# Kernel tuning notes

Measured on AMD Instinct MI355X. Metric: run time of the kernel, lower is better.

Reference implementation:

```python
import jax, jax.numpy as jnp
import numpy as np

B, H, Wd, CIN = 4, 64, 64, 65   # batch, height, width, in_channels (incl. time)
COUT = 256                      # out_channels (incl. time)
K = 3
KK = K * K
PAD, STRIDE = 1, 1
SOUT = 4                        # output_stabilizer_size (C4 rotations)
CURV = 1.0                      # Lorentz manifold curvature k
LIN_FEAT = (CIN - 1) * KK + 1   # 577


def make_c4_z2_indices(ksize):
    # (out_rotation, in_stabilizer=1, u, v, [s, u_src, v_src]) index table,
    # realizing the C4 filter rotation as a gather (as in GrouPy).
    f = np.arange(ksize * ksize).reshape(ksize, ksize)
    inds = np.zeros((4, 1, ksize, ksize, 3), dtype=np.int64)
    for r in range(4):
        rot = np.rot90(f, r)
        u, v = np.unravel_index(rot, (ksize, ksize))
        inds[r, 0, :, :, 1] = u
        inds[r, 0, :, :, 2] = v
    return inds

INDS = make_c4_z2_indices(K)


def setup_inputs() -> dict:
    key = jax.random.key(0)
    k1, k2, k3 = jax.random.split(key, 3)
    stdv = float(np.sqrt(2.0 / ((CIN - 1) * KK)))  # reset_parameters
    x = jax.random.normal(k1, (B, H, Wd, CIN), dtype=jnp.float32)
    W = jax.random.uniform(k2, (COUT, LIN_FEAT), minval=-stdv, maxval=stdv, dtype=jnp.float32)
    b = jax.random.uniform(k3, (COUT,), minval=-stdv, maxval=stdv, dtype=jnp.float32)
    return {"x": x, "W": W, "b": b}


def _unfold(x):
    # x: (B, C, H, W) -> (B, C*KK, Ho*Wo) in torch.nn.Unfold layout (channel-major, kernel-minor)
    xp = jnp.pad(x, ((0, 0), (0, 0), (PAD, PAD), (PAD, PAD)))
    ho = (H + 2 * PAD - K) // STRIDE + 1
    wo = (Wd + 2 * PAD - K) // STRIDE + 1
    cols = [xp[:, :, i:i + ho * STRIDE:STRIDE, j:j + wo * STRIDE:STRIDE]
            for i in range(K) for j in range(K)]
    p = jnp.stack(cols, axis=2)  # (B, C, KK, ho, wo)
    return p.reshape(B, CIN * KK, ho * wo), ho, wo


def _forward(x, W, b):
    # torch code does x.view(B, C, H, W) on channel-last data: a reshape, not a permute.
    xv = x.reshape(B, CIN, H, Wd)
    patches, ho, wo = _unfold(xv)
    patches = jnp.transpose(patches, (0, 2, 1))          # (B, P, C*KK)
    P = patches.shape[1]
    patches = patches.reshape(B, P, CIN, 1, K, K)
    patches = jnp.broadcast_to(patches, (B, P, CIN, SOUT, K, K))  # repeat over group dim
    # --- group-equivariant filter transform realized as a gather on patches ---
    ir = INDS.reshape(-1, 3)                              # (SOUT*KK, 3)
    pi = patches[:, :, :, ir[:, 0], ir[:, 1], ir[:, 2]]   # (B, P, C, SOUT*KK)
    pi = pi.reshape(B, P, CIN, SOUT, KK)
    pt = jnp.transpose(pi, (3, 0, 1, 2, 4)).reshape(SOUT, B, P, CIN * KK)
    # --- extract_lorentz_patches (vectorized over group dim) ---
    sqrt_k = jnp.sqrt(jnp.float32(CURV))
    t = jnp.maximum(pt[..., :KK], sqrt_k)                 # clamp time components
    t_resc = jnp.sqrt(jnp.sum(t * t, axis=-1, keepdims=True) - (KK - 1) * CURV)
    sp = pt[..., KK:]                                     # (SOUT,B,P,(C-1)*KK) channel-major
    sp = sp.reshape(SOUT, B, P, CIN - 1, KK).swapaxes(-1, -2).reshape(SOUT, B, P, (CIN - 1) * KK)
    pre = jnp.concatenate([t_resc, sp], axis=-1)          # (SOUT,B,P,LIN_FEAT)
    # --- LorentzFullyConnected: linear, then recompute time from space norm ---
    y = jnp.einsum('gbpf,of->gbpo', pre, W) + b           # (SOUT,B,P,COUT)
    y_sp = y[..., 1:]
    y_t = jnp.sqrt(jnp.sum(y_sp * y_sp, axis=-1, keepdims=True) + CURV)
    out = jnp.concatenate([y_t, y_sp], axis=-1)
    out = jnp.transpose(out, (1, 0, 2, 3)).reshape(B, SOUT, ho, wo, COUT)
    return out


def reference(x, W, b):
    return _forward(x, W, b)
```

## Files before the change

kernel.cpp:

```cpp
#include <hip/hip_runtime.h>
#include <hip/hip_bf16.h>

#define CIN 65
#define LIN 577
#define NSTEP 18
#define M_  16384

typedef __bf16 bf16x8 __attribute__((ext_vector_type(8)));
typedef float  f32x4  __attribute__((ext_vector_type(4)));
typedef unsigned short u16x8 __attribute__((ext_vector_type(8)));

__constant__ int SIG[4][9] = {
  {0,1,2,3,4,5,6,7,8},
  {2,5,8,1,4,7,0,3,6},
  {8,7,6,5,4,3,2,1,0},
  {6,3,0,7,4,1,8,5,2}};

__device__ __forceinline__ int swzm(int r) { return (r ^ (r >> 2)) & 3; }

__global__ __launch_bounds__(512) void prep_k(const float* __restrict__ x,
                                              const float* __restrict__ W,
                                              __hip_bfloat16* __restrict__ A,
                                              __hip_bfloat16* __restrict__ Wg,
                                              float* __restrict__ T) {
  __shared__ float lds[CIN * 3 * 72];
  const int tid = threadIdx.x;
  if (blockIdx.x >= 256) {
    int pidx = (blockIdx.x - 256) * 512 + tid;
    int jc  = pidx & 3;
    int col = (pidx >> 2) & 255;
    int t   = pidx >> 10;
    int ks  = t % NSTEP, g = t / NSTEP;
    int k   = SIG[(4 - g) & 3][ks >> 1];
    const float* src = W + col * LIN + 1 + k * 64 + (ks & 1) * 32 + jc * 8;
    u16x8 pk;
#pragma unroll
    for (int e = 0; e < 8; ++e) {
      union { __hip_bfloat16 h; unsigned short u; } cv;
      cv.h = __float2bfloat16(src[e]);
      pk[e] = cv.u;
    }
    *(u16x8*)(Wg + (size_t)pidx * 8) = pk;
    return;
  }
  const int b = blockIdx.x >> 6, py = blockIdx.x & 63;
  const float* xb = x + (size_t)b * (CIN * 4096);
  for (int i = tid; i < CIN * 3 * 18; i += 512)
    *(f32x4*)&lds[i * 4] = (f32x4){0.f, 0.f, 0.f, 0.f};
  __syncthreads();
  for (int i = tid; i < CIN * 3 * 16; i += 512) {
    int pr = i >> 4, j = i & 15;
    int c = pr / 3, dy = pr - c * 3;
    int hy = py + dy - 1;
    if (hy >= 0 && hy < 64)
      *(f32x4*)&lds[c * 216 + dy * 72 + 4 + j * 4] =
          *(const f32x4*)(xb + c * 4096 + hy * 64 + j * 4);
  }
  __syncthreads();

  const int wave = tid >> 6, px = tid & 63;
  const int rowid = (blockIdx.x << 6) | px;
#pragma unroll
  for (int qi = 0; qi < 9; ++qi) {
    int q = wave * 9 + qi;
    int m = q >> 3, cb8 = q & 7;
    int dy = m / 3, dx = m - dy * 3;
    const float* src = &lds[(1 + cb8 * 8) * 216 + dy * 72 + 3 + dx + px];
    u16x8 pk;
#pragma unroll
    for (int e = 0; e < 8; ++e) {
      union { __hip_bfloat16 h; unsigned short u; } cv;
      cv.h = __float2bfloat16(src[e * 216]);
      pk[e] = cv.u;
    }
    *(u16x8*)(A + ((size_t)q * M_ + rowid) * 8) = pk;
  }
  if (wave == 0) {
    float s = 0.f;
#pragma unroll
    for (int m = 0; m < 9; ++m) {
      float t = fmaxf(lds[(m / 3) * 72 + 3 + (m % 3) + px], 1.f);
      s += t * t;
    }
    T[rowid] = sqrtf(s - 8.f);
  }
}

__device__ __forceinline__ void async_cp16(const void* g, void* ldsbase) {
  __builtin_amdgcn_global_load_lds(
      (const __attribute__((address_space(1))) void*)g,
      (__attribute__((address_space(3))) void*)ldsbase, 16, 0, 0);
}

__global__ __launch_bounds__(512, 4) void gemm_k(const __hip_bfloat16* __restrict__ A,
                                                 const __hip_bfloat16* __restrict__ Wg,
                                                 const float* __restrict__ W,
                                                 const float* __restrict__ bias,
                                                 const float* __restrict__ T,
                                                 float* __restrict__ out) {
  __shared__ __align__(16) char smem[51712];
  const int fid = blockIdx.x;
  const int lid = ((fid & 7) << 6) | (fid >> 3);
  const int g = lid & 3, rb = lid >> 2;
  const int brow = rb << 7;
  const int tid = threadIdx.x, wave = tid >> 6, lane = tid & 63;
  const int fr = lane & 15, fq = lane >> 4;
  const int wr = (wave >> 2) * 64, wcb = (wave & 3) * 64;

  float* Tsh = (float*)(smem + 49152);
  float* Ps  = (float*)(smem + 49664);
  if (tid < 128) Tsh[tid] = T[brow + tid];

  const int bcol0 = tid >> 2, blc0 = (tid & 3) ^ swzm(bcol0);
  const int bcol1 = 128 + (tid >> 2), blc1 = (tid & 3) ^ swzm(bcol1);
  const __hip_bfloat16* Wgg = Wg + ((size_t)(g * NSTEP) << 13);
  auto STAGE_B = [&](char* pb, int ks) {
    const __hip_bfloat16* bs = Wgg + ((size_t)ks << 13);
    async_cp16(bs + bcol0 * 32 + blc0 * 8, pb + wave * 1024);
    async_cp16(bs + bcol1 * 32 + blc1 * 8, pb + wave * 1024 + 8192);
  };

  const __hip_bfloat16* Arow = A + (((size_t)fq * M_ + brow + wr + fr) << 3);
  auto LOAD_A = [&](bf16x8* dst, int ks) {
#pragma unroll
    for (int i = 0; i < 4; ++i)
      dst[i] = *(const bf16x8*)(Arow + (size_t)ks * (M_ * 32) + i * 128);
  };

  f32x4 acc[4][4] = {};
  auto COMPUTE = [&](const char* Bb, const bf16x8* af) {
    bf16x8 bf[4];
#pragma unroll
    for (int j = 0; j < 4; ++j) {
      int c = wcb + j * 16 + fr;
      bf[j] = *(const bf16x8*)(Bb + c * 64 + ((fq ^ swzm(c)) << 4));
    }
    __builtin_amdgcn_s_setprio(1);
#pragma unroll
    for (int i = 0; i < 4; ++i)
#pragma unroll
      for (int j = 0; j < 4; ++j)
        acc[i][j] = __builtin_amdgcn_mfma_f32_16x16x32_bf16(af[i], bf[j], acc[i][j], 0, 0, 0);
    __builtin_amdgcn_s_setprio(0);
  };

  bf16x8 afA[4], afB[4];
  char *cB = smem, *nB = smem + 16384, *tB = smem + 32768;
  STAGE_B(cB, 0);
  STAGE_B(nB, 1);
  LOAD_A(afA, 0);

  for (int kp = 0; kp < NSTEP; kp += 2) {
    asm volatile("s_waitcnt vmcnt(6)" ::: "memory");
    __builtin_amdgcn_s_barrier();
    if (kp + 2 < NSTEP) STAGE_B(tB, kp + 2);
    LOAD_A(afB, kp + 1);
    COMPUTE(cB, afA);
    { char* r = cB; cB = nB; nB = tB; tB = r; }
    if (kp + 1 < NSTEP - 1) {
      asm volatile("s_waitcnt vmcnt(6)" ::: "memory");
    } else {
      asm volatile("s_waitcnt vmcnt(4)" ::: "memory");
    }
    __builtin_amdgcn_s_barrier();
    if (kp + 3 < NSTEP) STAGE_B(tB, kp + 3);
    if (kp + 2 < NSTEP) LOAD_A(afA, kp + 2);
    COMPUTE(cB, afB);
    { char* r = cB; cB = nB; nB = tB; tB = r; }
  }
  __syncthreads();

  float bo[4], w0v[4]; int oc[4];
#pragma unroll
  for (int j = 0; j < 4; ++j) {
    oc[j]  = wcb + j * 16 + fr;
    bo[j]  = bias[oc[j]];
    w0v[j] = W[oc[j] * LIN];
  }
#pragma unroll
  for (int i = 0; i < 4; ++i) {
#pragma unroll
    for (int rr = 0; rr < 4; ++rr) {
      int rl = wr + i * 16 + fq * 4 + rr;
      int row = brow + rl;
      size_t obase = ((size_t)(((row >> 12) * 4 + g) * 4096 + (row & 4095)) << 8);
      float tval = Tsh[rl];
      float s = 0.f;
#pragma unroll
      for (int j = 0; j < 4; ++j) {
        float y = acc[i][j][rr] + bo[j] + tval * w0v[j];
        if (oc[j] != 0) { s += y * y; out[obase + oc[j]] = y; }
      }
      s += __shfl_xor(s, 1); s += __shfl_xor(s, 2);
      s += __shfl_xor(s, 4); s += __shfl_xor(s, 8);
      if (fr == 0) Ps[rl * 4 + (wave & 3)] = s;
    }
  }
  __syncthreads();
  if (tid < 128) {
    int row = brow + tid;
    float s = Ps[tid * 4] + Ps[tid * 4 + 1] + Ps[tid * 4 + 2] + Ps[tid * 4 + 3] + 1.0f;
    out[(size_t)(((row >> 12) * 4 + g) * 4096 + (row & 4095)) << 8] = sqrtf(s);
  }
}

extern "C" void kernel_launch(void* const* d_in, const int* in_sizes, int n_in,
                              void* d_out, int out_size, void* d_ws, size_t ws_size,
                              hipStream_t stream) {
  const float* x    = (const float*)d_in[0];
  const float* W    = (const float*)d_in[1];
  const float* bias = (const float*)d_in[2];
  float* out = (float*)d_out;

  char* ws = (char*)d_ws;
  __hip_bfloat16* Wg = (__hip_bfloat16*)ws;
  float*          T  = (float*)(ws + 1179648);
  __hip_bfloat16* A  = (__hip_bfloat16*)(ws + 1245184);

  prep_k<<<400, 512, 0, stream>>>(x, W, A, Wg, T);
  gemm_k<<<512, 512, 0, stream>>>(A, Wg, W, bias, T, out);
}
```

Before: 43.86 us.

## Shrink GEMM tile to 64 rows with 256-thread blocks and double buffering

Restructures the GEMM kernel from 128x256 tiles with 8 waves and triple-buffered B to 64x256 tiles with 4 waves, double-buffered B and a simpler single-step loop. The grid doubles to 1024 blocks in a plain group-major order without the previous block-index swizzle, and T is read from global memory instead of staged in LDS. The aim is more blocks and occupancy with less LDS per block, at the cost of reloading B twice as often per row and exposing more A-load latency because A is no longer prefetched a step ahead.

```diff
diff --git a/kernel.cpp b/kernel.cpp
--- a/kernel.cpp
+++ b/kernel.cpp
@@ -92,43 +92,40 @@
       (__attribute__((address_space(3))) void*)ldsbase, 16, 0, 0);
 }
 
-__global__ __launch_bounds__(512, 4) void gemm_k(const __hip_bfloat16* __restrict__ A,
+__global__ __launch_bounds__(256, 4) void gemm_k(const __hip_bfloat16* __restrict__ A,
                                                  const __hip_bfloat16* __restrict__ Wg,
                                                  const float* __restrict__ W,
                                                  const float* __restrict__ bias,
                                                  const float* __restrict__ T,
                                                  float* __restrict__ out) {
-  __shared__ __align__(16) char smem[51712];
-  const int fid = blockIdx.x;
-  const int lid = ((fid & 7) << 6) | (fid >> 3);
-  const int g = lid & 3, rb = lid >> 2;
-  const int brow = rb << 7;
+  __shared__ __align__(16) char smem[32768];
+  const int g = blockIdx.x >> 8, rb = blockIdx.x & 255;
+  const int brow = rb << 6;
   const int tid = threadIdx.x, wave = tid >> 6, lane = tid & 63;
   const int fr = lane & 15, fq = lane >> 4;
-  const int wr = (wave >> 2) * 64, wcb = (wave & 3) * 64;
-
-  float* Tsh = (float*)(smem + 49152);
-  float* Ps  = (float*)(smem + 49664);
-  if (tid < 128) Tsh[tid] = T[brow + tid];
-
-  const int bcol0 = tid >> 2, blc0 = (tid & 3) ^ swzm(bcol0);
-  const int bcol1 = 128 + (tid >> 2), blc1 = (tid & 3) ^ swzm(bcol1);
+  const int wcb = wave * 64;
+
+  const int bc  = tid >> 2;
   const __hip_bfloat16* Wgg = Wg + ((size_t)(g * NSTEP) << 13);
   auto STAGE_B = [&](char* pb, int ks) {
     const __hip_bfloat16* bs = Wgg + ((size_t)ks << 13);
-    async_cp16(bs + bcol0 * 32 + blc0 * 8, pb + wave * 1024);
-    async_cp16(bs + bcol1 * 32 + blc1 * 8, pb + wave * 1024 + 8192);
+#pragma unroll
+    for (int l = 0; l < 4; ++l) {
+      int c = l * 64 + bc;
+      int lc = (tid & 3) ^ swzm(c);
+      async_cp16(bs + c * 32 + lc * 8, pb + (l * 256 + wave * 64) * 16);
+    }
   };
-
-  const __hip_bfloat16* Arow = A + (((size_t)fq * M_ + brow + wr + fr) << 3);
-  auto LOAD_A = [&](bf16x8* dst, int ks) {
+  const __hip_bfloat16* Alane = A + (((size_t)fq * M_ + brow + fr) << 3);
+  bf16x8 af[4];
+  auto LOAD_A = [&](int ks) {
 #pragma unroll
     for (int i = 0; i < 4; ++i)
-      dst[i] = *(const bf16x8*)(Arow + (size_t)ks * (M_ * 32) + i * 128);
+      af[i] = *(const bf16x8*)(Alane + (size_t)ks * (M_ * 32) + i * 128);
   };
 
   f32x4 acc[4][4] = {};
-  auto COMPUTE = [&](const char* Bb, const bf16x8* af) {
+  auto COMPUTE = [&](const char* Bb) {
     bf16x8 bf[4];
 #pragma unroll
     for (int j = 0; j < 4; ++j) {
@@ -144,32 +141,17 @@
     __builtin_amdgcn_s_setprio(0);
   };
 
-  bf16x8 afA[4], afB[4];
-  char *cB = smem, *nB = smem + 16384, *tB = smem + 32768;
-  STAGE_B(cB, 0);
-  STAGE_B(nB, 1);
-  LOAD_A(afA, 0);
-
-  for (int kp = 0; kp < NSTEP; kp += 2) {
-    asm volatile("s_waitcnt vmcnt(6)" ::: "memory");
+  STAGE_B(smem, 0);
+  for (int ks = 0; ks < NSTEP; ++ks) {
+    LOAD_A(ks);
+    asm volatile("s_waitcnt vmcnt(4)" ::: "memory");
     __builtin_amdgcn_s_barrier();
-    if (kp + 2 < NSTEP) STAGE_B(tB, kp + 2);
-    LOAD_A(afB, kp + 1);
-    COMPUTE(cB, afA);
-    { char* r = cB; cB = nB; nB = tB; tB = r; }
-    if (kp + 1 < NSTEP - 1) {
-      asm volatile("s_waitcnt vmcnt(6)" ::: "memory");
-    } else {
-      asm volatile("s_waitcnt vmcnt(4)" ::: "memory");
-    }
-    __builtin_amdgcn_s_barrier();
-    if (kp + 3 < NSTEP) STAGE_B(tB, kp + 3);
-    if (kp + 2 < NSTEP) LOAD_A(afA, kp + 2);
-    COMPUTE(cB, afB);
-    { char* r = cB; cB = nB; nB = tB; tB = r; }
-  }
-  __syncthreads();
-
+    if (ks + 1 < NSTEP) STAGE_B(smem + ((ks + 1) & 1) * 16384, ks + 1);
+    COMPUTE(smem + (ks & 1) * 16384);
+  }
+  __syncthreads();
+
+  float* Ps = (float*)smem;
   float bo[4], w0v[4]; int oc[4];
 #pragma unroll
   for (int j = 0; j < 4; ++j) {
@@ -181,10 +163,10 @@
   for (int i = 0; i < 4; ++i) {
 #pragma unroll
     for (int rr = 0; rr < 4; ++rr) {
-      int rl = wr + i * 16 + fq * 4 + rr;
+      int rl = i * 16 + fq * 4 + rr;
       int row = brow + rl;
       size_t obase = ((size_t)(((row >> 12) * 4 + g) * 4096 + (row & 4095)) << 8);
-      float tval = Tsh[rl];
+      float tval = T[row];
       float s = 0.f;
 #pragma unroll
       for (int j = 0; j < 4; ++j) {
@@ -193,11 +175,11 @@
       }
       s += __shfl_xor(s, 1); s += __shfl_xor(s, 2);
       s += __shfl_xor(s, 4); s += __shfl_xor(s, 8);
-      if (fr == 0) Ps[rl * 4 + (wave & 3)] = s;
-    }
-  }
-  __syncthreads();
-  if (tid < 128) {
+      if (fr == 0) Ps[rl * 4 + wave] = s;
+    }
+  }
+  __syncthreads();
+  if (tid < 64) {
     int row = brow + tid;
     float s = Ps[tid * 4] + Ps[tid * 4 + 1] + Ps[tid * 4 + 2] + Ps[tid * 4 + 3] + 1.0f;
     out[(size_t)(((row >> 12) * 4 + g) * 4096 + (row & 4095)) << 8] = sqrtf(s);
@@ -218,5 +200,5 @@
   __hip_bfloat16* A  = (__hip_bfloat16*)(ws + 1245184);
 
   prep_k<<<400, 512, 0, stream>>>(x, W, A, Wg, T);
-  gemm_k<<<512, 512, 0, stream>>>(A, Wg, W, bias, T, out);
-}
+  gemm_k<<<1024, 256, 0, stream>>>(A, Wg, W, bias, T, out);
+}
```

Measured after the change: 46.33 us. 1.06x slower.
